# Kernel tuning notes

Measured on AMD Instinct MI355X. Metric: run time of the kernel, lower is better.

## Reference

```python
import math
import jax, jax.numpy as jnp
import numpy as np

N_HEAD = 16
ROPE_BASE = 10000.0


def _rope_tables(T, half, dtype):
    # build_sin_cos(seq_len, dim=head_dim//2): inv freq of length `half`
    pos = jnp.arange(T, dtype=jnp.float32)[:, None]                       # (T,1)
    inv = jnp.exp(jnp.arange(0, 2 * half, 2, dtype=jnp.float32) * (-math.log(ROPE_BASE) / (2 * half)))
    ang = pos * inv                                                        # (T, half)
    return jnp.sin(ang).astype(dtype), jnp.cos(ang).astype(dtype)


def _apply_rope(q, k, sin, cos):
    # q,k: (B,T,H,Dh); sin,cos: (T, Dh//2) -> broadcast over batch and heads
    half = q.shape[-1] // 2
    s = sin[None, :, None, :]
    c = cos[None, :, None, :]
    q1, q2 = q[..., :half], q[..., half:]
    k1, k2 = k[..., :half], k[..., half:]
    q = jnp.concatenate([q1 * c - q2 * s, q2 * c + q1 * s], axis=-1)
    k = jnp.concatenate([k1 * c - k2 * s, k2 * c + k1 * s], axis=-1)
    return q, k


def setup_inputs() -> dict:
    key = jax.random.key(0)
    k1, k2, k3 = jax.random.split(key, 3)
    B, T, C = 2, 2048, 2048
    x = jax.random.normal(k1, (B, T, C), dtype=jnp.float32)
    w_qkv = jax.random.normal(k2, (3 * C, C), dtype=jnp.float32) * (1.0 / math.sqrt(C))
    w_proj = jax.random.normal(k3, (C, C), dtype=jnp.float32) * (1.0 / math.sqrt(C))
    return {"x": x, "w_qkv": w_qkv, "w_proj": w_proj}


def reference(x, w_qkv, w_proj):
    B, T, C = x.shape
    H = N_HEAD
    Dh = C // H
    # fused QKV projection (Linear, no bias): (B,T,3C) -> (B,T,3,H,Dh)
    qkv = jnp.einsum('btc,oc->bto', x, w_qkv).reshape(B, T, 3, H, Dh)
    q, k, v = qkv[:, :, 0], qkv[:, :, 1], qkv[:, :, 2]          # (B,T,H,Dh)
    sin, cos = _rope_tables(T, Dh // 2, x.dtype)
    q, k = _apply_rope(q, k, sin, cos)
    # causal attention, scale 1/sqrt(Dh) (flash default softmax_scale=None)
    scale = 1.0 / math.sqrt(Dh)
    scores = jnp.einsum('bqhd,bkhd->bhqk', q, k) * scale        # (B,H,T,T)
    mask = jnp.tril(jnp.ones((T, T), dtype=bool))
    scores = jnp.where(mask[None, None], scores, jnp.finfo(scores.dtype).min)
    probs = jax.nn.softmax(scores, axis=-1)
    out = jnp.einsum('bhqk,bkhd->bqhd', probs, v)               # (B,T,H,Dh)
    # faithful to original: permute(0,2,1,3) then reshape_as(x)
    out = jnp.transpose(out, (0, 2, 1, 3)).reshape(B, T, C)
    return jnp.einsum('btc,oc->bto', out, w_proj)
```

## Files before the change

kernel.cpp:

```cpp
#include <hip/hip_runtime.h>
#include <hip/hip_bf16.h>

typedef __bf16 bf16_t;
typedef __bf16 bf16x8 __attribute__((ext_vector_type(8)));
typedef __bf16 bf16x4 __attribute__((ext_vector_type(4)));
typedef float f32x4 __attribute__((ext_vector_type(4)));
typedef float f32x16 __attribute__((ext_vector_type(16)));
typedef unsigned u32x4v __attribute__((ext_vector_type(4)));

#define MFMA16(a, b, c) __builtin_amdgcn_mfma_f32_16x16x32_bf16(a, b, c, 0, 0, 0)
#define MFMA32(a, b, c) __builtin_amdgcn_mfma_f32_32x32x16_bf16(a, b, c, 0, 0, 0)

__device__ __forceinline__ void async_copy16(const void* g, void* l) {
  __builtin_amdgcn_global_load_lds(
      (const __attribute__((address_space(1))) void*)g,
      (__attribute__((address_space(3))) void*)l, 16, 0, 0);
}

__device__ __forceinline__ unsigned cvtpk(float lo, float hi) {
  unsigned r;
  asm("v_cvt_pk_bf16_f32 %0, %1, %2" : "=v"(r) : "v"(lo), "v"(hi));
  return r;
}

__global__ void cast_all(const float* __restrict__ x, const float* __restrict__ wqkv,
                         const float* __restrict__ wproj, bf16_t* __restrict__ xb,
                         bf16_t* __restrict__ wqkvb, bf16_t* __restrict__ wprojb) {
  int stride = gridDim.x * blockDim.x;
  for (int i = blockIdx.x * blockDim.x + threadIdx.x; i < 3145728; i += stride) {
    const float* src;
    bf16_t* dst;
    int idx;
    if (i < 1048576) { src = x; dst = xb; idx = i; }
    else if (i < 2621440) { src = wqkv; dst = wqkvb; idx = i - 1048576; }
    else { src = wproj; dst = wprojb; idx = i - 2621440; }
    const float* p = src + (size_t)idx * 8;
    f32x4 a = *(const f32x4*)p;
    f32x4 b = *(const f32x4*)(p + 4);
    bf16x8 o;
    o[0] = (bf16_t)a[0]; o[1] = (bf16_t)a[1]; o[2] = (bf16_t)a[2]; o[3] = (bf16_t)a[3];
    o[4] = (bf16_t)b[0]; o[5] = (bf16_t)b[1]; o[6] = (bf16_t)b[2]; o[7] = (bf16_t)b[3];
    *(bf16x8*)(dst + (size_t)idx * 8) = o;
  }
}

__global__ __launch_bounds__(512, 2) void gemm_qkv(
    const bf16_t* __restrict__ A, const bf16_t* __restrict__ Bw,
    bf16_t* __restrict__ qo, bf16_t* __restrict__ ko,
    int K) {
  __shared__ __align__(16) char lds[131072];
  int tid = threadIdx.x;
  int w = tid >> 6, lane = tid & 63;
  int wm = w & 1, wn = w >> 1;
  int mr = lane & 15, kg = lane >> 4;

  int orig = blockIdx.x;
  int chunk = orig & 7, i = orig >> 3;
  int by = (chunk & 3) * 4 + (i & 3);
  int bx = (chunk >> 2) * 8 + (i >> 2);
  int row0 = by * 256, col0 = bx * 256;

  int lr = tid >> 3, ch = (tid & 7) ^ (lr & 7);
  size_t aoff[4], boff[4];
#pragma unroll
  for (int g = 0; g < 4; ++g) {
    int gr = g * 32 + (lr & 31) + (lr >> 5) * 128;
    aoff[g] = (size_t)(row0 + gr) * K + ch * 8;
  }
#pragma unroll
  for (int p = 0; p < 4; ++p) {
    int gr = (lr >> 4) * 64 + p * 16 + (lr & 15);
    boff[p] = (size_t)(col0 + gr) * K + ch * 8;
  }

  auto stgA = [&](int q, int g, int kt) {
    async_copy16(A + aoff[g] + kt * 64, lds + q * 65536 + g * 8192 + tid * 16);
  };
  auto stgB = [&](int q, int p, int kt) {
    async_copy16(Bw + boff[p] + kt * 64, lds + q * 65536 + 32768 + p * 8192 + tid * 16);
  };

  f32x4 zero = {0.f, 0.f, 0.f, 0.f};
  f32x4 acc[8][4];
#pragma unroll
  for (int mi = 0; mi < 8; ++mi)
#pragma unroll
    for (int ni = 0; ni < 4; ++ni) acc[mi][ni] = zero;

  int nt = K >> 6;

  stgB(0, 0, 0); stgB(0, 1, 0); stgB(0, 2, 0); stgB(0, 3, 0);
  stgA(0, 0, 0); stgA(0, 1, 0); stgA(0, 2, 0); stgA(0, 3, 0);
  asm volatile("s_waitcnt vmcnt(0)" ::: "memory");
  __builtin_amdgcn_sched_barrier(0);
  __builtin_amdgcn_s_barrier();
  __builtin_amdgcn_sched_barrier(0);

#pragma unroll 1
  for (int t = 0; t < nt; ++t) {
    int q = t & 1, qn = q ^ 1;
    int kt = (t + 1 < nt) ? (t + 1) : t;
    const char* Ab = lds + q * 65536;
    const char* Bb = Ab + 32768;
    bf16x8 bf[4][2];

#define QKV_PHASE(MI0, STG, DOWAIT)                                             \
    {                                                                           \
      int r0 = ((MI0) >> 1) * 64 + wm * 32 + mr;                                \
      int r1 = r0 + 16;                                                         \
      bf16x8 a00 = *(const bf16x8*)(Ab + r0 * 128 + ((kg * 16) ^ ((r0 & 7) << 4)));      \
      bf16x8 a01 = *(const bf16x8*)(Ab + r0 * 128 + ((64 + kg * 16) ^ ((r0 & 7) << 4))); \
      bf16x8 a10 = *(const bf16x8*)(Ab + r1 * 128 + ((kg * 16) ^ ((r1 & 7) << 4)));      \
      bf16x8 a11 = *(const bf16x8*)(Ab + r1 * 128 + ((64 + kg * 16) ^ ((r1 & 7) << 4))); \
      STG;                                                                      \
      __builtin_amdgcn_sched_barrier(0);                                        \
      if (DOWAIT) { asm volatile("s_waitcnt vmcnt(4)" ::: "memory"); }          \
      __builtin_amdgcn_s_barrier();                                             \
      asm volatile("s_waitcnt lgkmcnt(0)" ::: "memory");                        \
      __builtin_amdgcn_sched_barrier(0);                                        \
      __builtin_amdgcn_s_setprio(1);                                            \
      _Pragma("unroll")                                                         \
      for (int ni = 0; ni < 4; ++ni) {                                          \
        acc[MI0][ni] = MFMA16(a00, bf[ni][0], acc[MI0][ni]);                    \
        acc[MI0][ni] = MFMA16(a01, bf[ni][1], acc[MI0][ni]);                    \
        acc[(MI0) + 1][ni] = MFMA16(a10, bf[ni][0], acc[(MI0) + 1][ni]);        \
        acc[(MI0) + 1][ni] = MFMA16(a11, bf[ni][1], acc[(MI0) + 1][ni]);        \
      }                                                                         \
      __builtin_amdgcn_s_setprio(0);                                            \
      __builtin_amdgcn_sched_barrier(0);                                        \
      __builtin_amdgcn_s_barrier();                                             \
      __builtin_amdgcn_sched_barrier(0);                                        \
    }

#pragma unroll
    for (int ni = 0; ni < 4; ++ni) {
      int rb = ni * 64 + wn * 16 + mr;
      bf[ni][0] = *(const bf16x8*)(Bb + rb * 128 + ((kg * 16) ^ ((rb & 7) << 4)));
      bf[ni][1] = *(const bf16x8*)(Bb + rb * 128 + ((64 + kg * 16) ^ ((rb & 7) << 4)));
    }
    QKV_PHASE(0, (stgA(qn, 0, kt), stgA(qn, 1, kt), stgB(qn, 0, kt), stgB(qn, 1, kt)), 1)
    QKV_PHASE(2, (stgA(qn, 2, kt), stgA(qn, 3, kt), stgB(qn, 2, kt), stgB(qn, 3, kt)), 0)
    QKV_PHASE(4, (void)0, 0)
    QKV_PHASE(6, (void)0, 0)
#undef QKV_PHASE
  }
  asm volatile("s_waitcnt vmcnt(0)" ::: "memory");
  __syncthreads();

  char* tb = &lds[0];
  int s = col0 >> 11;
  int h0 = (col0 >> 7) & 15;
  int b = row0 >> 11, t0 = row0 & 2047;
#pragma unroll
  for (int mi = 0; mi < 8; ++mi)
#pragma unroll
    for (int ni = 0; ni < 4; ++ni)
#pragma unroll
      for (int jj = 0; jj < 4; ++jj) {
        int rl = wm * 128 + mi * 16 + kg * 4 + jj;
        int cb = (wn * 64 + ni * 16 + mr) * 2;
        *(bf16_t*)(tb + rl * 512 + (cb ^ ((rl & 7) << 4))) = (bf16_t)acc[mi][ni][jj];
      }
  __syncthreads();
  int r = tid >> 1, hs = tid & 1;
  const char* rowb = tb + r * 512;
  int sz = (r & 7) << 4;
  int t = t0 + r;
  bf16_t* dst = (s == 0 ? qo : ko) + ((size_t)((b * 16 + h0 + hs) * 2048 + t)) * 128;
  float tf = (float)t;
  const float cinv = -0.20762050593046014f;
  float postm = (s == 0) ? 0.12751744f : 1.0f;
  bf16x8 vin[16];
#pragma unroll
  for (int m = 0; m < 16; ++m)
    vin[m] = *(const bf16x8*)(rowb + ((hs * 256 + m * 16) ^ sz));
#pragma unroll
  for (int m = 0; m < 8; ++m) {
    bf16x8 o1, o2;
#pragma unroll
    for (int e = 0; e < 8; ++e) {
      float ang = tf * exp2f((float)(m * 8 + e) * cinv);
      float sv = __sinf(ang), cv = __cosf(ang);
      float x1 = (float)vin[m][e], x2 = (float)vin[m + 8][e];
      o1[e] = (bf16_t)((x1 * cv - x2 * sv) * postm);
      o2[e] = (bf16_t)((x2 * cv + x1 * sv) * postm);
    }
    *(bf16x8*)(dst + m * 8) = o1;
    *(bf16x8*)(dst + 64 + m * 8) = o2;
  }
}

template <int MODE>
__global__ __launch_bounds__(512, 2) void gemm256(
    const bf16_t* __restrict__ A, const bf16_t* __restrict__ Bw, float* __restrict__ C,
    bf16_t* __restrict__ vto, int M, int N, int K, int nby, int colbase) {
  __shared__ __align__(16) char lds[147456];
  int tid = threadIdx.x;
  int w = tid >> 6, lane = tid & 63;
  int wm = w >> 1, wn = w & 1;
  int mr = lane & 15, kg = lane >> 4;

  int nwg = gridDim.x;
  int orig = blockIdx.x;
  int wgid = (orig & 7) * (nwg >> 3) + (orig >> 3);
  int by = wgid % nby, bx = wgid / nby;
  int row0 = by * 256, col0 = colbase + bx * 128;

  size_t aoff[4], boff[2];
#pragma unroll
  for (int it = 0; it < 4; ++it) {
    int c = tid + it * 512;
    int r = c >> 3;
    int chs = (c & 7) ^ (r & 7);
    aoff[it] = (size_t)(row0 + r) * K + chs * 8;
  }
#pragma unroll
  for (int it = 0; it < 2; ++it) {
    int c = tid + it * 512;
    int r = c >> 3;
    int chs = (c & 7) ^ (r & 7);
    boff[it] = (size_t)(col0 - colbase + r) * K + chs * 8;
  }

  auto stageA = [&](int buf, int kt, int half) {
    char* Ad = &lds[buf * 49152];
#pragma unroll
    for (int it = half * 2; it < half * 2 + 2; ++it)
      async_copy16(A + aoff[it] + kt * 64, Ad + (tid + it * 512) * 16);
  };
  auto stageB = [&](int buf, int kt) {
    char* Bd = &lds[buf * 49152 + 32768];
#pragma unroll
    for (int it = 0; it < 2; ++it)
      async_copy16(Bw + boff[it] + kt * 64, Bd + (tid + it * 512) * 16);
  };

  f32x4 zero = {0.f, 0.f, 0.f, 0.f};
  f32x4 acc[4][4];
#pragma unroll
  for (int mi = 0; mi < 4; ++mi)
#pragma unroll
    for (int ni = 0; ni < 4; ++ni) acc[mi][ni] = zero;

  int nt = K >> 6;
  stageA(0, 0, 0); stageA(0, 0, 1); stageB(0, 0);
  stageA(1, 1, 0); stageA(1, 1, 1); stageB(1, 1);
  asm volatile("s_waitcnt vmcnt(6)" ::: "memory");
  __builtin_amdgcn_sched_barrier(0);
  __builtin_amdgcn_s_barrier();
  __builtin_amdgcn_sched_barrier(0);

#pragma unroll 1
  for (int t = 0; t < nt; ++t) {
    int cur = t % 3;
    int nxt = (t + 2) % 3;
    int kt2 = (t + 2 < nt) ? (t + 2) : t;
    const char* Ab = &lds[cur * 49152];
    const char* Bb = &lds[cur * 49152 + 32768];
    bf16x8 af[4][2], bfr[4][2];
#pragma unroll
    for (int mi = 0; mi < 4; ++mi) {
      int row = wm * 64 + mi * 16 + mr;
      const char* rb = Ab + row * 128;
      int sz = (row & 7) << 4;
      af[mi][0] = *(const bf16x8*)(rb + ((kg * 16) ^ sz));
      af[mi][1] = *(const bf16x8*)(rb + ((64 + kg * 16) ^ sz));
    }
#pragma unroll
    for (int ni = 0; ni < 4; ++ni) {
      int row = wn * 64 + ni * 16 + mr;
      const char* rb = Bb + row * 128;
      int sz = (row & 7) << 4;
      bfr[ni][0] = *(const bf16x8*)(rb + ((kg * 16) ^ sz));
      bfr[ni][1] = *(const bf16x8*)(rb + ((64 + kg * 16) ^ sz));
    }
    stageA(nxt, kt2, 0);
    __builtin_amdgcn_s_setprio(1);
#pragma unroll
    for (int mi = 0; mi < 4; ++mi) {
      acc[mi][0] = MFMA16(af[mi][0], bfr[0][0], acc[mi][0]);
      acc[mi][0] = MFMA16(af[mi][1], bfr[0][1], acc[mi][0]);
    }
    __builtin_amdgcn_s_setprio(0);
    stageA(nxt, kt2, 1);
    __builtin_amdgcn_s_setprio(1);
#pragma unroll
    for (int mi = 0; mi < 4; ++mi) {
      acc[mi][1] = MFMA16(af[mi][0], bfr[1][0], acc[mi][1]);
      acc[mi][1] = MFMA16(af[mi][1], bfr[1][1], acc[mi][1]);
    }
    __builtin_amdgcn_s_setprio(0);
    stageB(nxt, kt2);
    __builtin_amdgcn_s_setprio(1);
#pragma unroll
    for (int mi = 0; mi < 4; ++mi) {
      acc[mi][2] = MFMA16(af[mi][0], bfr[2][0], acc[mi][2]);
      acc[mi][2] = MFMA16(af[mi][1], bfr[2][1], acc[mi][2]);
      acc[mi][3] = MFMA16(af[mi][0], bfr[3][0], acc[mi][3]);
      acc[mi][3] = MFMA16(af[mi][1], bfr[3][1], acc[mi][3]);
    }
    __builtin_amdgcn_s_setprio(0);
    asm volatile("s_waitcnt vmcnt(6)" ::: "memory");
    __builtin_amdgcn_sched_barrier(0);
    __builtin_amdgcn_s_barrier();
    __builtin_amdgcn_sched_barrier(0);
  }
  asm volatile("s_waitcnt vmcnt(0)" ::: "memory");
  __syncthreads();

  if (MODE == 0) {
#pragma unroll
    for (int mi = 0; mi < 4; ++mi)
#pragma unroll
      for (int ni = 0; ni < 4; ++ni)
#pragma unroll
        for (int jj = 0; jj < 4; ++jj) {
          int row = row0 + wm * 64 + mi * 16 + kg * 4 + jj;
          int col = col0 + wn * 64 + ni * 16 + mr;
          C[(size_t)row * N + col] = acc[mi][ni][jj];
        }
  } else {
    char* tb = &lds[0];
    int h = (col0 >> 7) & 15;
    int b = row0 >> 11, t0 = row0 & 2047;
#pragma unroll
    for (int mi = 0; mi < 4; ++mi)
#pragma unroll
      for (int ni = 0; ni < 4; ++ni)
#pragma unroll
        for (int jj = 0; jj < 4; ++jj) {
          int rloc = wm * 64 + mi * 16 + kg * 4 + jj;
          int cloc = wn * 64 + ni * 16 + mr;
          *(bf16_t*)(tb + cloc * 512 + ((rloc * 2) ^ ((cloc & 7) << 4))) =
              (bf16_t)acc[mi][ni][jj];
        }
    __syncthreads();
    int d = tid >> 2, qt = tid & 3;
    const char* rowb = tb + d * 512;
    int sz = (d & 7) << 4;
    bf16_t* dst = vto + ((size_t)((b * 16 + h) * 128 + d)) * 2048 + t0 + qt * 64;
#pragma unroll
    for (int m2 = 0; m2 < 8; ++m2)
      *(bf16x8*)(dst + m2 * 8) = *(const bf16x8*)(rowb + ((qt * 128 + m2 * 16) ^ sz));
  }
}

__global__ __launch_bounds__(256, 2) void attn_kernel(
    const bf16_t* __restrict__ qg, const bf16_t* __restrict__ kgl,
    const bf16_t* __restrict__ vtg, bf16_t* __restrict__ og) {
  __shared__ __align__(16) bf16_t Ks[2][64 * 128];
  __shared__ __align__(16) bf16_t Vs[2][128 * 64];
  const int T = 2048;
  int tid = threadIdx.x;
  int w = tid >> 6, lane = tid & 63;
  int l31 = lane & 31, hi = lane >> 5;

  int L = blockIdx.x;
  int halfg = L >> 8;
  int Lr = L & 255;
  int role = (Lr & 7) * 32 + (Lr >> 3);
  int bx = role & 7, bh = role >> 3;
  int qb = halfg ? bx : (15 - bx);

  const bf16_t* Q = qg + (size_t)bh * T * 128;
  const bf16_t* K = kgl + (size_t)bh * T * 128;
  const bf16_t* Vt = vtg + (size_t)bh * 128 * T;

  int sb = tid * 16;
  int krl = sb >> 8;
  int kc = (sb & 255) ^ (krl << 4);
  size_t ksrc = (size_t)krl * 128 + (kc >> 1);
  int vdl = sb >> 7;
  int vc = (sb & 127) ^ ((vdl & 7) << 4);
  size_t vsrc = (size_t)vdl * 2048 + (vc >> 1);

  auto stage = [&](int buf, int kb) {
#pragma unroll
    for (int it = 0; it < 4; ++it)
      async_copy16(K + (size_t)(kb + it * 16) * 128 + ksrc, &Ks[buf][it * 2048 + tid * 8]);
#pragma unroll
    for (int it = 0; it < 4; ++it)
      async_copy16(Vt + (size_t)it * 65536 + kb + vsrc, &Vs[buf][it * 2048 + tid * 8]);
  };

  int b = bh >> 4, h = bh & 15;
  f32x16 zero16 = {0.f};
  int swzK = (l31 & 15) << 4;
  int swzV = (l31 & 7) << 4;

  int qw0 = qb * 128 + w * 32;
  int tq = qw0 + l31;
  const bf16_t* qrow = Q + (size_t)tq * 128 + hi * 8;
  bf16x8 qf[8];
#pragma unroll
  for (int dc = 0; dc < 8; ++dc) qf[dc] = *(const bf16x8*)(qrow + dc * 16);

  f32x16 acc[4];
#pragma unroll
  for (int dt = 0; dt < 4; ++dt) acc[dt] = zero16;
  float mrun = -1e30f, lpart = 0.f;

  int nj = 2 * qb + 2;
  stage(0, 0);
  stage(1, 64);
#pragma unroll 1
  for (int j = 0; j < nj; ++j) {
    int cur = j & 1;
    if (j + 1 < nj) {
      asm volatile("s_waitcnt vmcnt(8)" ::: "memory");
    } else {
      asm volatile("s_waitcnt vmcnt(0)" ::: "memory");
    }
    __builtin_amdgcn_sched_barrier(0);
    __syncthreads();
    int kb = j * 64;
    if (kb <= qw0) {
      const char* KsB = (const char*)&Ks[cur][0];
      const char* VsB = (const char*)&Vs[cur][0];
      f32x16 s0 = zero16, s1 = zero16;
      __builtin_amdgcn_s_setprio(1);
#pragma unroll
      for (int dc = 0; dc < 8; ++dc) {
        int cb = dc * 32 + hi * 16;
        bf16x8 k0 = *(const bf16x8*)(KsB + l31 * 256 + (cb ^ swzK));
        bf16x8 k1 = *(const bf16x8*)(KsB + (32 + l31) * 256 + (cb ^ swzK));
        s0 = MFMA32(k0, qf[dc], s0);
        s1 = MFMA32(k1, qf[dc], s1);
      }
      __builtin_amdgcn_s_setprio(0);
      float p0[16], p1[16];
      float lmax = -3e38f;
      bool diag = (kb + 63 > qw0);
#pragma unroll
      for (int r = 0; r < 16; ++r) {
        int kk = (r & 3) + 8 * (r >> 2) + 4 * hi;
        float v0 = s0[r], v1 = s1[r];
        if (diag) {
          if (kb + kk > tq) v0 = -1e30f;
          if (kb + 32 + kk > tq) v1 = -1e30f;
        }
        p0[r] = v0; p1[r] = v1;
        lmax = fmaxf(lmax, fmaxf(v0, v1));
      }
      bool ok = (lmax <= mrun + 8.0f);
      if (!__all(ok)) {
        float tmax = fmaxf(lmax, __shfl_xor(lmax, 32, 64));
        float mn = fmaxf(mrun, tmax);
        float corr = __builtin_amdgcn_exp2f(mrun - mn);
        mrun = mn;
        lpart *= corr;
#pragma unroll
        for (int dt = 0; dt < 4; ++dt)
#pragma unroll
          for (int r = 0; r < 16; ++r) acc[dt][r] *= corr;
      }
#pragma unroll
      for (int r = 0; r < 16; ++r) {
        float e0 = __builtin_amdgcn_exp2f(p0[r] - mrun);
        float e1 = __builtin_amdgcn_exp2f(p1[r] - mrun);
        p0[r] = e0; p1[r] = e1;
        lpart += e0 + e1;
      }
      bf16x8 pa0, pa1, pa2, pa3;
#define BUILD_PA(dst, P, B0)                                         \
      { unsigned a0 = cvtpk(P[(B0) + 0], P[(B0) + 1]);               \
        unsigned a1 = cvtpk(P[(B0) + 2], P[(B0) + 3]);               \
        unsigned b0 = cvtpk(P[(B0) + 4], P[(B0) + 5]);               \
        unsigned b1 = cvtpk(P[(B0) + 6], P[(B0) + 7]);               \
        unsigned xa0 = __shfl_xor(a0, 32, 64);                       \
        unsigned xa1 = __shfl_xor(a1, 32, 64);                       \
        unsigned xb0 = __shfl_xor(b0, 32, 64);                       \
        unsigned xb1 = __shfl_xor(b1, 32, 64);                       \
        u32x4v fw;                                                   \
        fw[0] = hi ? xb0 : a0; fw[1] = hi ? xb1 : a1;                \
        fw[2] = hi ? b0 : xa0; fw[3] = hi ? b1 : xa1;                \
        dst = __builtin_bit_cast(bf16x8, fw); }
      BUILD_PA(pa0, p0, 0)
      BUILD_PA(pa1, p0, 8)
      BUILD_PA(pa2, p1, 0)
      BUILD_PA(pa3, p1, 8)
#undef BUILD_PA
      __builtin_amdgcn_s_setprio(1);
#pragma unroll
      for (int dt = 0; dt < 4; ++dt) {
        const char* vrow = VsB + (dt * 32 + l31) * 128;
        bf16x8 v0 = *(const bf16x8*)(vrow + ((hi * 16) ^ swzV));
        bf16x8 v1 = *(const bf16x8*)(vrow + ((32 + hi * 16) ^ swzV));
        bf16x8 v2 = *(const bf16x8*)(vrow + ((64 + hi * 16) ^ swzV));
        bf16x8 v3 = *(const bf16x8*)(vrow + ((96 + hi * 16) ^ swzV));
        acc[dt] = MFMA32(v0, pa0, acc[dt]);
        acc[dt] = MFMA32(v1, pa1, acc[dt]);
        acc[dt] = MFMA32(v2, pa2, acc[dt]);
        acc[dt] = MFMA32(v3, pa3, acc[dt]);
      }
      __builtin_amdgcn_s_setprio(0);
    }
    __syncthreads();
    if (j + 2 < nj) stage(cur, (j + 2) * 64);
  }
  float l = lpart + __shfl_xor(lpart, 32, 64);
  float invl = 1.0f / l;
  size_t orow_idx = (size_t)b * 2048 + h * 128 + (tq >> 4);
  bf16_t* orow = og + orow_idx * 2048 + (tq & 15) * 128;
#pragma unroll
  for (int dt = 0; dt < 4; ++dt)
#pragma unroll
    for (int g = 0; g < 4; ++g) {
      bf16x4 v4;
#pragma unroll
      for (int e = 0; e < 4; ++e) v4[e] = (bf16_t)(acc[dt][4 * g + e] * invl);
      *(bf16x4*)(orow + dt * 32 + 8 * g + 4 * hi) = v4;
    }
}

extern "C" void kernel_launch(void* const* d_in, const int* in_sizes, int n_in,
                              void* d_out, int out_size, void* d_ws, size_t ws_size,
                              hipStream_t stream) {
  const float* x = (const float*)d_in[0];
  const float* wqkv = (const float*)d_in[1];
  const float* wproj = (const float*)d_in[2];
  float* out = (float*)d_out;
  char* ws = (char*)d_ws;

  const size_t OFF_WQKV = 16777216;
  const size_t OFF_WPROJ = 41943040;
  const size_t OFF_Q = 50331648;
  const size_t OFF_K = 67108864;
  const size_t OFF_VT = 83886080;

  bf16_t* xb = (bf16_t*)(ws);
  bf16_t* wqkvb = (bf16_t*)(ws + OFF_WQKV);
  bf16_t* wprojb = (bf16_t*)(ws + OFF_WPROJ);
  bf16_t* g_q = (bf16_t*)(ws + OFF_Q);
  bf16_t* g_k = (bf16_t*)(ws + OFF_K);
  bf16_t* g_vt = (bf16_t*)(ws + OFF_VT);
  bf16_t* g_att = (bf16_t*)(ws);

  cast_all<<<4096, 256, 0, stream>>>(x, wqkv, wproj, xb, wqkvb, wprojb);
  gemm_qkv<<<256, 512, 0, stream>>>(xb, wqkvb, g_q, g_k, 2048);
  gemm256<1><<<256, 512, 0, stream>>>(xb, wqkvb + (size_t)4096 * 2048, nullptr, g_vt,
                                      4096, 2048, 2048, 16, 4096);
  attn_kernel<<<512, 256, 0, stream>>>(g_q, g_k, g_vt, g_att);
  gemm256<0><<<256, 512, 0, stream>>>(g_att, wprojb, out, nullptr, 4096, 2048, 2048, 16, 0);
}
```

Measured before the change: 243.3 us.

## Merge QK-rope GEMM and V-transpose GEMM into one fused launch

Combines the Q/K projection kernel (with RoPE epilogue) and the V projection kernel (with transposed store) into a single 512-block launch that branches on block index. This removes one kernel launch and the tail/idle gap between the two GEMMs, letting the V blocks fill CUs left idle by the QK grid. The fused kernel uses 147KB LDS and launch bounds of 1 block per CU, so occupancy follows the larger footprint and the two paths now share register allocation.

```diff
diff --git a/kernel.cpp b/kernel.cpp
--- a/kernel.cpp
+++ b/kernel.cpp
@@ -44,282 +44,261 @@
   }
 }
 
-__global__ __launch_bounds__(512, 2) void gemm_qkv(
+__global__ __launch_bounds__(512, 1) void gemm_fused(
     const bf16_t* __restrict__ A, const bf16_t* __restrict__ Bw,
-    bf16_t* __restrict__ qo, bf16_t* __restrict__ ko,
+    bf16_t* __restrict__ qo, bf16_t* __restrict__ ko, bf16_t* __restrict__ vto,
     int K) {
-  __shared__ __align__(16) char lds[131072];
-  int tid = threadIdx.x;
-  int w = tid >> 6, lane = tid & 63;
-  int wm = w & 1, wn = w >> 1;
-  int mr = lane & 15, kg = lane >> 4;
-
-  int orig = blockIdx.x;
-  int chunk = orig & 7, i = orig >> 3;
-  int by = (chunk & 3) * 4 + (i & 3);
-  int bx = (chunk >> 2) * 8 + (i >> 2);
-  int row0 = by * 256, col0 = bx * 256;
-
-  int lr = tid >> 3, ch = (tid & 7) ^ (lr & 7);
-  size_t aoff[4], boff[4];
-#pragma unroll
-  for (int g = 0; g < 4; ++g) {
-    int gr = g * 32 + (lr & 31) + (lr >> 5) * 128;
-    aoff[g] = (size_t)(row0 + gr) * K + ch * 8;
-  }
-#pragma unroll
-  for (int p = 0; p < 4; ++p) {
-    int gr = (lr >> 4) * 64 + p * 16 + (lr & 15);
-    boff[p] = (size_t)(col0 + gr) * K + ch * 8;
-  }
-
-  auto stgA = [&](int q, int g, int kt) {
-    async_copy16(A + aoff[g] + kt * 64, lds + q * 65536 + g * 8192 + tid * 16);
-  };
-  auto stgB = [&](int q, int p, int kt) {
-    async_copy16(Bw + boff[p] + kt * 64, lds + q * 65536 + 32768 + p * 8192 + tid * 16);
-  };
-
-  f32x4 zero = {0.f, 0.f, 0.f, 0.f};
-  f32x4 acc[8][4];
-#pragma unroll
-  for (int mi = 0; mi < 8; ++mi)
-#pragma unroll
-    for (int ni = 0; ni < 4; ++ni) acc[mi][ni] = zero;
-
-  int nt = K >> 6;
-
-  stgB(0, 0, 0); stgB(0, 1, 0); stgB(0, 2, 0); stgB(0, 3, 0);
-  stgA(0, 0, 0); stgA(0, 1, 0); stgA(0, 2, 0); stgA(0, 3, 0);
-  asm volatile("s_waitcnt vmcnt(0)" ::: "memory");
-  __builtin_amdgcn_sched_barrier(0);
-  __builtin_amdgcn_s_barrier();
-  __builtin_amdgcn_sched_barrier(0);
-
-#pragma unroll 1
-  for (int t = 0; t < nt; ++t) {
-    int q = t & 1, qn = q ^ 1;
-    int kt = (t + 1 < nt) ? (t + 1) : t;
-    const char* Ab = lds + q * 65536;
-    const char* Bb = Ab + 32768;
-    bf16x8 bf[4][2];
-
-#define QKV_PHASE(MI0, STG, DOWAIT)                                             \
-    {                                                                           \
-      int r0 = ((MI0) >> 1) * 64 + wm * 32 + mr;                                \
-      int r1 = r0 + 16;                                                         \
-      bf16x8 a00 = *(const bf16x8*)(Ab + r0 * 128 + ((kg * 16) ^ ((r0 & 7) << 4)));      \
-      bf16x8 a01 = *(const bf16x8*)(Ab + r0 * 128 + ((64 + kg * 16) ^ ((r0 & 7) << 4))); \
-      bf16x8 a10 = *(const bf16x8*)(Ab + r1 * 128 + ((kg * 16) ^ ((r1 & 7) << 4)));      \
-      bf16x8 a11 = *(const bf16x8*)(Ab + r1 * 128 + ((64 + kg * 16) ^ ((r1 & 7) << 4))); \
-      STG;                                                                      \
-      __builtin_amdgcn_sched_barrier(0);                                        \
-      if (DOWAIT) { asm volatile("s_waitcnt vmcnt(4)" ::: "memory"); }          \
-      __builtin_amdgcn_s_barrier();                                             \
-      asm volatile("s_waitcnt lgkmcnt(0)" ::: "memory");                        \
-      __builtin_amdgcn_sched_barrier(0);                                        \
-      __builtin_amdgcn_s_setprio(1);                                            \
-      _Pragma("unroll")                                                         \
-      for (int ni = 0; ni < 4; ++ni) {                                          \
-        acc[MI0][ni] = MFMA16(a00, bf[ni][0], acc[MI0][ni]);                    \
-        acc[MI0][ni] = MFMA16(a01, bf[ni][1], acc[MI0][ni]);                    \
-        acc[(MI0) + 1][ni] = MFMA16(a10, bf[ni][0], acc[(MI0) + 1][ni]);        \
-        acc[(MI0) + 1][ni] = MFMA16(a11, bf[ni][1], acc[(MI0) + 1][ni]);        \
-      }                                                                         \
-      __builtin_amdgcn_s_setprio(0);                                            \
-      __builtin_amdgcn_sched_barrier(0);                                        \
-      __builtin_amdgcn_s_barrier();                                             \
-      __builtin_amdgcn_sched_barrier(0);                                        \
-    }
-
-#pragma unroll
-    for (int ni = 0; ni < 4; ++ni) {
-      int rb = ni * 64 + wn * 16 + mr;
-      bf[ni][0] = *(const bf16x8*)(Bb + rb * 128 + ((kg * 16) ^ ((rb & 7) << 4)));
-      bf[ni][1] = *(const bf16x8*)(Bb + rb * 128 + ((64 + kg * 16) ^ ((rb & 7) << 4)));
-    }
-    QKV_PHASE(0, (stgA(qn, 0, kt), stgA(qn, 1, kt), stgB(qn, 0, kt), stgB(qn, 1, kt)), 1)
-    QKV_PHASE(2, (stgA(qn, 2, kt), stgA(qn, 3, kt), stgB(qn, 2, kt), stgB(qn, 3, kt)), 0)
-    QKV_PHASE(4, (void)0, 0)
-    QKV_PHASE(6, (void)0, 0)
-#undef QKV_PHASE
-  }
-  asm volatile("s_waitcnt vmcnt(0)" ::: "memory");
-  __syncthreads();
-
-  char* tb = &lds[0];
-  int s = col0 >> 11;
-  int h0 = (col0 >> 7) & 15;
-  int b = row0 >> 11, t0 = row0 & 2047;
-#pragma unroll
-  for (int mi = 0; mi < 8; ++mi)
-#pragma unroll
-    for (int ni = 0; ni < 4; ++ni)
-#pragma unroll
-      for (int jj = 0; jj < 4; ++jj) {
-        int rl = wm * 128 + mi * 16 + kg * 4 + jj;
-        int cb = (wn * 64 + ni * 16 + mr) * 2;
-        *(bf16_t*)(tb + rl * 512 + (cb ^ ((rl & 7) << 4))) = (bf16_t)acc[mi][ni][jj];
-      }
-  __syncthreads();
-  int r = tid >> 1, hs = tid & 1;
-  const char* rowb = tb + r * 512;
-  int sz = (r & 7) << 4;
-  int t = t0 + r;
-  bf16_t* dst = (s == 0 ? qo : ko) + ((size_t)((b * 16 + h0 + hs) * 2048 + t)) * 128;
-  float tf = (float)t;
-  const float cinv = -0.20762050593046014f;
-  float postm = (s == 0) ? 0.12751744f : 1.0f;
-  bf16x8 vin[16];
-#pragma unroll
-  for (int m = 0; m < 16; ++m)
-    vin[m] = *(const bf16x8*)(rowb + ((hs * 256 + m * 16) ^ sz));
-#pragma unroll
-  for (int m = 0; m < 8; ++m) {
-    bf16x8 o1, o2;
-#pragma unroll
-    for (int e = 0; e < 8; ++e) {
-      float ang = tf * exp2f((float)(m * 8 + e) * cinv);
-      float sv = __sinf(ang), cv = __cosf(ang);
-      float x1 = (float)vin[m][e], x2 = (float)vin[m + 8][e];
-      o1[e] = (bf16_t)((x1 * cv - x2 * sv) * postm);
-      o2[e] = (bf16_t)((x2 * cv + x1 * sv) * postm);
-    }
-    *(bf16x8*)(dst + m * 8) = o1;
-    *(bf16x8*)(dst + 64 + m * 8) = o2;
-  }
-}
-
-template <int MODE>
-__global__ __launch_bounds__(512, 2) void gemm256(
-    const bf16_t* __restrict__ A, const bf16_t* __restrict__ Bw, float* __restrict__ C,
-    bf16_t* __restrict__ vto, int M, int N, int K, int nby, int colbase) {
   __shared__ __align__(16) char lds[147456];
   int tid = threadIdx.x;
   int w = tid >> 6, lane = tid & 63;
-  int wm = w >> 1, wn = w & 1;
   int mr = lane & 15, kg = lane >> 4;
-
-  int nwg = gridDim.x;
-  int orig = blockIdx.x;
-  int wgid = (orig & 7) * (nwg >> 3) + (orig >> 3);
-  int by = wgid % nby, bx = wgid / nby;
-  int row0 = by * 256, col0 = colbase + bx * 128;
-
-  size_t aoff[4], boff[2];
-#pragma unroll
-  for (int it = 0; it < 4; ++it) {
-    int c = tid + it * 512;
-    int r = c >> 3;
-    int chs = (c & 7) ^ (r & 7);
-    aoff[it] = (size_t)(row0 + r) * K + chs * 8;
-  }
-#pragma unroll
-  for (int it = 0; it < 2; ++it) {
-    int c = tid + it * 512;
-    int r = c >> 3;
-    int chs = (c & 7) ^ (r & 7);
-    boff[it] = (size_t)(col0 - colbase + r) * K + chs * 8;
-  }
-
-  auto stageA = [&](int buf, int kt, int half) {
-    char* Ad = &lds[buf * 49152];
-#pragma unroll
-    for (int it = half * 2; it < half * 2 + 2; ++it)
-      async_copy16(A + aoff[it] + kt * 64, Ad + (tid + it * 512) * 16);
-  };
-  auto stageB = [&](int buf, int kt) {
-    char* Bd = &lds[buf * 49152 + 32768];
-#pragma unroll
-    for (int it = 0; it < 2; ++it)
-      async_copy16(Bw + boff[it] + kt * 64, Bd + (tid + it * 512) * 16);
-  };
-
-  f32x4 zero = {0.f, 0.f, 0.f, 0.f};
-  f32x4 acc[4][4];
-#pragma unroll
-  for (int mi = 0; mi < 4; ++mi)
-#pragma unroll
-    for (int ni = 0; ni < 4; ++ni) acc[mi][ni] = zero;
-
-  int nt = K >> 6;
-  stageA(0, 0, 0); stageA(0, 0, 1); stageB(0, 0);
-  stageA(1, 1, 0); stageA(1, 1, 1); stageB(1, 1);
-  asm volatile("s_waitcnt vmcnt(6)" ::: "memory");
-  __builtin_amdgcn_sched_barrier(0);
-  __builtin_amdgcn_s_barrier();
-  __builtin_amdgcn_sched_barrier(0);
+  int bid = blockIdx.x;
+
+  if (bid < 256) {
+    int wm = w & 1, wn = w >> 1;
+    int chunk = bid & 7, i = bid >> 3;
+    int by = (chunk & 3) * 4 + (i & 3);
+    int bx = (chunk >> 2) * 8 + (i >> 2);
+    int row0 = by * 256, col0 = bx * 256;
+
+    int lr = tid >> 3, ch = (tid & 7) ^ (lr & 7);
+    size_t aoff[4], boff[4];
+#pragma unroll
+    for (int g = 0; g < 4; ++g) {
+      int gr = g * 32 + (lr & 31) + (lr >> 5) * 128;
+      aoff[g] = (size_t)(row0 + gr) * K + ch * 8;
+    }
+#pragma unroll
+    for (int p = 0; p < 4; ++p) {
+      int gr = (lr >> 4) * 64 + p * 16 + (lr & 15);
+      boff[p] = (size_t)(col0 + gr) * K + ch * 8;
+    }
+
+    auto stgA = [&](int q, int g, int kt) {
+      async_copy16(A + aoff[g] + kt * 64, lds + q * 65536 + g * 8192 + tid * 16);
+    };
+    auto stgB = [&](int q, int p, int kt) {
+      async_copy16(Bw + boff[p] + kt * 64, lds + q * 65536 + 32768 + p * 8192 + tid * 16);
+    };
+
+    f32x4 zero = {0.f, 0.f, 0.f, 0.f};
+    f32x4 acc[8][4];
+#pragma unroll
+    for (int mi = 0; mi < 8; ++mi)
+#pragma unroll
+      for (int ni = 0; ni < 4; ++ni) acc[mi][ni] = zero;
+
+    int nt = K >> 6;
+
+    stgB(0, 0, 0); stgB(0, 1, 0); stgB(0, 2, 0); stgB(0, 3, 0);
+    stgA(0, 0, 0); stgA(0, 1, 0); stgA(0, 2, 0); stgA(0, 3, 0);
+    asm volatile("s_waitcnt vmcnt(0)" ::: "memory");
+    __builtin_amdgcn_sched_barrier(0);
+    __builtin_amdgcn_s_barrier();
+    __builtin_amdgcn_sched_barrier(0);
 
 #pragma unroll 1
-  for (int t = 0; t < nt; ++t) {
-    int cur = t % 3;
-    int nxt = (t + 2) % 3;
-    int kt2 = (t + 2 < nt) ? (t + 2) : t;
-    const char* Ab = &lds[cur * 49152];
-    const char* Bb = &lds[cur * 49152 + 32768];
-    bf16x8 af[4][2], bfr[4][2];
-#pragma unroll
-    for (int mi = 0; mi < 4; ++mi) {
-      int row = wm * 64 + mi * 16 + mr;
-      const char* rb = Ab + row * 128;
-      int sz = (row & 7) << 4;
-      af[mi][0] = *(const bf16x8*)(rb + ((kg * 16) ^ sz));
-      af[mi][1] = *(const bf16x8*)(rb + ((64 + kg * 16) ^ sz));
-    }
-#pragma unroll
-    for (int ni = 0; ni < 4; ++ni) {
-      int row = wn * 64 + ni * 16 + mr;
-      const char* rb = Bb + row * 128;
-      int sz = (row & 7) << 4;
-      bfr[ni][0] = *(const bf16x8*)(rb + ((kg * 16) ^ sz));
-      bfr[ni][1] = *(const bf16x8*)(rb + ((64 + kg * 16) ^ sz));
-    }
-    stageA(nxt, kt2, 0);
-    __builtin_amdgcn_s_setprio(1);
-#pragma unroll
-    for (int mi = 0; mi < 4; ++mi) {
-      acc[mi][0] = MFMA16(af[mi][0], bfr[0][0], acc[mi][0]);
-      acc[mi][0] = MFMA16(af[mi][1], bfr[0][1], acc[mi][0]);
-    }
-    __builtin_amdgcn_s_setprio(0);
-    stageA(nxt, kt2, 1);
-    __builtin_amdgcn_s_setprio(1);
-#pragma unroll
-    for (int mi = 0; mi < 4; ++mi) {
-      acc[mi][1] = MFMA16(af[mi][0], bfr[1][0], acc[mi][1]);
-      acc[mi][1] = MFMA16(af[mi][1], bfr[1][1], acc[mi][1]);
-    }
-    __builtin_amdgcn_s_setprio(0);
-    stageB(nxt, kt2);
-    __builtin_amdgcn_s_setprio(1);
-#pragma unroll
-    for (int mi = 0; mi < 4; ++mi) {
-      acc[mi][2] = MFMA16(af[mi][0], bfr[2][0], acc[mi][2]);
-      acc[mi][2] = MFMA16(af[mi][1], bfr[2][1], acc[mi][2]);
-      acc[mi][3] = MFMA16(af[mi][0], bfr[3][0], acc[mi][3]);
-      acc[mi][3] = MFMA16(af[mi][1], bfr[3][1], acc[mi][3]);
-    }
-    __builtin_amdgcn_s_setprio(0);
+    for (int t = 0; t < nt; ++t) {
+      int q = t & 1, qn = q ^ 1;
+      int kt = (t + 1 < nt) ? (t + 1) : t;
+      const char* Ab = lds + q * 65536;
+      const char* Bb = Ab + 32768;
+      bf16x8 bf[4][2];
+
+#define QKV_PHASE(MI0, STG, DOWAIT)                                             \
+      {                                                                         \
+        int r0 = ((MI0) >> 1) * 64 + wm * 32 + mr;                              \
+        int r1 = r0 + 16;                                                       \
+        bf16x8 a00 = *(const bf16x8*)(Ab + r0 * 128 + ((kg * 16) ^ ((r0 & 7) << 4)));      \
+        bf16x8 a01 = *(const bf16x8*)(Ab + r0 * 128 + ((64 + kg * 16) ^ ((r0 & 7) << 4))); \
+        bf16x8 a10 = *(const bf16x8*)(Ab + r1 * 128 + ((kg * 16) ^ ((r1 & 7) << 4)));      \
+        bf16x8 a11 = *(const bf16x8*)(Ab + r1 * 128 + ((64 + kg * 16) ^ ((r1 & 7) << 4))); \
+        STG;                                                                    \
+        __builtin_amdgcn_sched_barrier(0);                                      \
+        if (DOWAIT) { asm volatile("s_waitcnt vmcnt(4)" ::: "memory"); }        \
+        __builtin_amdgcn_s_barrier();                                           \
+        asm volatile("s_waitcnt lgkmcnt(0)" ::: "memory");                      \
+        __builtin_amdgcn_sched_barrier(0);                                      \
+        __builtin_amdgcn_s_setprio(1);                                          \
+        _Pragma("unroll")                                                       \
+        for (int ni = 0; ni < 4; ++ni) {                                        \
+          acc[MI0][ni] = MFMA16(a00, bf[ni][0], acc[MI0][ni]);                  \
+          acc[MI0][ni] = MFMA16(a01, bf[ni][1], acc[MI0][ni]);                  \
+          acc[(MI0) + 1][ni] = MFMA16(a10, bf[ni][0], acc[(MI0) + 1][ni]);      \
+          acc[(MI0) + 1][ni] = MFMA16(a11, bf[ni][1], acc[(MI0) + 1][ni]);      \
+        }                                                                       \
+        __builtin_amdgcn_s_setprio(0);                                          \
+        __builtin_amdgcn_sched_barrier(0);                                      \
+        __builtin_amdgcn_s_barrier();                                           \
+        __builtin_amdgcn_sched_barrier(0);                                      \
+      }
+
+#pragma unroll
+      for (int ni = 0; ni < 4; ++ni) {
+        int rb = ni * 64 + wn * 16 + mr;
+        bf[ni][0] = *(const bf16x8*)(Bb + rb * 128 + ((kg * 16) ^ ((rb & 7) << 4)));
+        bf[ni][1] = *(const bf16x8*)(Bb + rb * 128 + ((64 + kg * 16) ^ ((rb & 7) << 4)));
+      }
+      QKV_PHASE(0, (stgA(qn, 0, kt), stgA(qn, 1, kt), stgB(qn, 0, kt), stgB(qn, 1, kt)), 1)
+      QKV_PHASE(2, (stgA(qn, 2, kt), stgA(qn, 3, kt), stgB(qn, 2, kt), stgB(qn, 3, kt)), 0)
+      QKV_PHASE(4, (void)0, 0)
+      QKV_PHASE(6, (void)0, 0)
+#undef QKV_PHASE
+    }
+    asm volatile("s_waitcnt vmcnt(0)" ::: "memory");
+    __syncthreads();
+
+    char* tb = &lds[0];
+    int s = col0 >> 11;
+    int h0 = (col0 >> 7) & 15;
+    int b = row0 >> 11, t0 = row0 & 2047;
+#pragma unroll
+    for (int mi = 0; mi < 8; ++mi)
+#pragma unroll
+      for (int ni = 0; ni < 4; ++ni)
+#pragma unroll
+        for (int jj = 0; jj < 4; ++jj) {
+          int rl = wm * 128 + mi * 16 + kg * 4 + jj;
+          int cb = (wn * 64 + ni * 16 + mr) * 2;
+          *(bf16_t*)(tb + rl * 512 + (cb ^ ((rl & 7) << 4))) = (bf16_t)acc[mi][ni][jj];
+        }
+    __syncthreads();
+    int r = tid >> 1, hs = tid & 1;
+    const char* rowb = tb + r * 512;
+    int sz = (r & 7) << 4;
+    int t = t0 + r;
+    bf16_t* dst = (s == 0 ? qo : ko) + ((size_t)((b * 16 + h0 + hs) * 2048 + t)) * 128;
+    float tf = (float)t;
+    const float cinv = -0.20762050593046014f;
+    float postm = (s == 0) ? 0.12751744f : 1.0f;
+    bf16x8 vin[16];
+#pragma unroll
+    for (int m = 0; m < 16; ++m)
+      vin[m] = *(const bf16x8*)(rowb + ((hs * 256 + m * 16) ^ sz));
+#pragma unroll
+    for (int m = 0; m < 8; ++m) {
+      bf16x8 o1, o2;
+#pragma unroll
+      for (int e = 0; e < 8; ++e) {
+        float ang = tf * exp2f((float)(m * 8 + e) * cinv);
+        float sv = __sinf(ang), cv = __cosf(ang);
+        float x1 = (float)vin[m][e], x2 = (float)vin[m + 8][e];
+        o1[e] = (bf16_t)((x1 * cv - x2 * sv) * postm);
+        o2[e] = (bf16_t)((x2 * cv + x1 * sv) * postm);
+      }
+      *(bf16x8*)(dst + m * 8) = o1;
+      *(bf16x8*)(dst + 64 + m * 8) = o2;
+    }
+  } else {
+    int wm = w >> 1, wn = w & 1;
+    const bf16_t* Bv = Bw + (size_t)4096 * K;
+    int vid = bid - 256;
+    int wgid = (vid & 7) * 32 + (vid >> 3);
+    int by = wgid % 16, bx = wgid / 16;
+    int row0 = by * 256, col0 = 4096 + bx * 128;
+
+    size_t aoff[4], boff[2];
+#pragma unroll
+    for (int it = 0; it < 4; ++it) {
+      int c = tid + it * 512;
+      int r = c >> 3;
+      int chs = (c & 7) ^ (r & 7);
+      aoff[it] = (size_t)(row0 + r) * K + chs * 8;
+    }
+#pragma unroll
+    for (int it = 0; it < 2; ++it) {
+      int c = tid + it * 512;
+      int r = c >> 3;
+      int chs = (c & 7) ^ (r & 7);
+      boff[it] = (size_t)(col0 - 4096 + r) * K + chs * 8;
+    }
+
+    auto stageA = [&](int buf, int kt, int half) {
+      char* Ad = &lds[buf * 49152];
+#pragma unroll
+      for (int it = half * 2; it < half * 2 + 2; ++it)
+        async_copy16(A + aoff[it] + kt * 64, Ad + (tid + it * 512) * 16);
+    };
+    auto stageB = [&](int buf, int kt) {
+      char* Bd = &lds[buf * 49152 + 32768];
+#pragma unroll
+      for (int it = 0; it < 2; ++it)
+        async_copy16(Bv + boff[it] + kt * 64, Bd + (tid + it * 512) * 16);
+    };
+
+    f32x4 zero = {0.f, 0.f, 0.f, 0.f};
+    f32x4 acc[4][4];
+#pragma unroll
+    for (int mi = 0; mi < 4; ++mi)
+#pragma unroll
+      for (int ni = 0; ni < 4; ++ni) acc[mi][ni] = zero;
+
+    int nt = K >> 6;
+    stageA(0, 0, 0); stageA(0, 0, 1); stageB(0, 0);
+    stageA(1, 1, 0); stageA(1, 1, 1); stageB(1, 1);
     asm volatile("s_waitcnt vmcnt(6)" ::: "memory");
     __builtin_amdgcn_sched_barrier(0);
     __builtin_amdgcn_s_barrier();
     __builtin_amdgcn_sched_barrier(0);
-  }
-  asm volatile("s_waitcnt vmcnt(0)" ::: "memory");
-  __syncthreads();
-
-  if (MODE == 0) {
-#pragma unroll
-    for (int mi = 0; mi < 4; ++mi)
-#pragma unroll
-      for (int ni = 0; ni < 4; ++ni)
-#pragma unroll
-        for (int jj = 0; jj < 4; ++jj) {
-          int row = row0 + wm * 64 + mi * 16 + kg * 4 + jj;
-          int col = col0 + wn * 64 + ni * 16 + mr;
-          C[(size_t)row * N + col] = acc[mi][ni][jj];
-        }
-  } else {
+
+#pragma unroll 1
+    for (int t = 0; t < nt; ++t) {
+      int cur = t % 3;
+      int nxt = (t + 2) % 3;
+      int kt2 = (t + 2 < nt) ? (t + 2) : t;
+      const char* Ab = &lds[cur * 49152];
+      const char* Bb = &lds[cur * 49152 + 32768];
+      bf16x8 af[4][2], bfr[4][2];
+#pragma unroll
+      for (int mi = 0; mi < 4; ++mi) {
+        int row = wm * 64 + mi * 16 + mr;
+        const char* rb = Ab + row * 128;
+        int sz = (row & 7) << 4;
+        af[mi][0] = *(const bf16x8*)(rb + ((kg * 16) ^ sz));
+        af[mi][1] = *(const bf16x8*)(rb + ((64 + kg * 16) ^ sz));
+      }
+#pragma unroll
+      for (int ni = 0; ni < 4; ++ni) {
+        int row = wn * 64 + ni * 16 + mr;
+        const char* rb = Bb + row * 128;
+        int sz = (row & 7) << 4;
+        bfr[ni][0] = *(const bf16x8*)(rb + ((kg * 16) ^ sz));
+        bfr[ni][1] = *(const bf16x8*)(rb + ((64 + kg * 16) ^ sz));
+      }
+      stageA(nxt, kt2, 0);
+      __builtin_amdgcn_s_setprio(1);
+#pragma unroll
+      for (int mi = 0; mi < 4; ++mi) {
+        acc[mi][0] = MFMA16(af[mi][0], bfr[0][0], acc[mi][0]);
+        acc[mi][0] = MFMA16(af[mi][1], bfr[0][1], acc[mi][0]);
+      }
+      __builtin_amdgcn_s_setprio(0);
+      stageA(nxt, kt2, 1);
+      __builtin_amdgcn_s_setprio(1);
+#pragma unroll
+      for (int mi = 0; mi < 4; ++mi) {
+        acc[mi][1] = MFMA16(af[mi][0], bfr[1][0], acc[mi][1]);
+        acc[mi][1] = MFMA16(af[mi][1], bfr[1][1], acc[mi][1]);
+      }
+      __builtin_amdgcn_s_setprio(0);
+      stageB(nxt, kt2);
+      __builtin_amdgcn_s_setprio(1);
+#pragma unroll
+      for (int mi = 0; mi < 4; ++mi) {
+        acc[mi][2] = MFMA16(af[mi][0], bfr[2][0], acc[mi][2]);
+        acc[mi][2] = MFMA16(af[mi][1], bfr[2][1], acc[mi][2]);
+        acc[mi][3] = MFMA16(af[mi][0], bfr[3][0], acc[mi][3]);
+        acc[mi][3] = MFMA16(af[mi][1], bfr[3][1], acc[mi][3]);
+      }
+      __builtin_amdgcn_s_setprio(0);
+      asm volatile("s_waitcnt vmcnt(6)" ::: "memory");
+      __builtin_amdgcn_sched_barrier(0);
+      __builtin_amdgcn_s_barrier();
+      __builtin_amdgcn_sched_barrier(0);
+    }
+    asm volatile("s_waitcnt vmcnt(0)" ::: "memory");
+    __syncthreads();
+
     char* tb = &lds[0];
     int h = (col0 >> 7) & 15;
     int b = row0 >> 11, t0 = row0 & 2047;
@@ -343,6 +322,135 @@
     for (int m2 = 0; m2 < 8; ++m2)
       *(bf16x8*)(dst + m2 * 8) = *(const bf16x8*)(rowb + ((qt * 128 + m2 * 16) ^ sz));
   }
+}
+
+__global__ __launch_bounds__(512, 2) void gemm256(
+    const bf16_t* __restrict__ A, const bf16_t* __restrict__ Bw, float* __restrict__ C,
+    int M, int N, int K, int nby) {
+  __shared__ __align__(16) char lds[147456];
+  int tid = threadIdx.x;
+  int w = tid >> 6, lane = tid & 63;
+  int wm = w >> 1, wn = w & 1;
+  int mr = lane & 15, kg = lane >> 4;
+
+  int nwg = gridDim.x;
+  int orig = blockIdx.x;
+  int wgid = (orig & 7) * (nwg >> 3) + (orig >> 3);
+  int by = wgid % nby, bx = wgid / nby;
+  int row0 = by * 256, col0 = bx * 128;
+
+  size_t aoff[4], boff[2];
+#pragma unroll
+  for (int it = 0; it < 4; ++it) {
+    int c = tid + it * 512;
+    int r = c >> 3;
+    int chs = (c & 7) ^ (r & 7);
+    aoff[it] = (size_t)(row0 + r) * K + chs * 8;
+  }
+#pragma unroll
+  for (int it = 0; it < 2; ++it) {
+    int c = tid + it * 512;
+    int r = c >> 3;
+    int chs = (c & 7) ^ (r & 7);
+    boff[it] = (size_t)(col0 + r) * K + chs * 8;
+  }
+
+  auto stageA = [&](int buf, int kt, int half) {
+    char* Ad = &lds[buf * 49152];
+#pragma unroll
+    for (int it = half * 2; it < half * 2 + 2; ++it)
+      async_copy16(A + aoff[it] + kt * 64, Ad + (tid + it * 512) * 16);
+  };
+  auto stageB = [&](int buf, int kt) {
+    char* Bd = &lds[buf * 49152 + 32768];
+#pragma unroll
+    for (int it = 0; it < 2; ++it)
+      async_copy16(Bw + boff[it] + kt * 64, Bd + (tid + it * 512) * 16);
+  };
+
+  f32x4 zero = {0.f, 0.f, 0.f, 0.f};
+  f32x4 acc[4][4];
+#pragma unroll
+  for (int mi = 0; mi < 4; ++mi)
+#pragma unroll
+    for (int ni = 0; ni < 4; ++ni) acc[mi][ni] = zero;
+
+  int nt = K >> 6;
+  stageA(0, 0, 0); stageA(0, 0, 1); stageB(0, 0);
+  stageA(1, 1, 0); stageA(1, 1, 1); stageB(1, 1);
+  asm volatile("s_waitcnt vmcnt(6)" ::: "memory");
+  __builtin_amdgcn_sched_barrier(0);
+  __builtin_amdgcn_s_barrier();
+  __builtin_amdgcn_sched_barrier(0);
+
+#pragma unroll 1
+  for (int t = 0; t < nt; ++t) {
+    int cur = t % 3;
+    int nxt = (t + 2) % 3;
+    int kt2 = (t + 2 < nt) ? (t + 2) : t;
+    const char* Ab = &lds[cur * 49152];
+    const char* Bb = &lds[cur * 49152 + 32768];
+    bf16x8 af[4][2], bfr[4][2];
+#pragma unroll
+    for (int mi = 0; mi < 4; ++mi) {
+      int row = wm * 64 + mi * 16 + mr;
+      const char* rb = Ab + row * 128;
+      int sz = (row & 7) << 4;
+      af[mi][0] = *(const bf16x8*)(rb + ((kg * 16) ^ sz));
+      af[mi][1] = *(const bf16x8*)(rb + ((64 + kg * 16) ^ sz));
+    }
+#pragma unroll
+    for (int ni = 0; ni < 4; ++ni) {
+      int row = wn * 64 + ni * 16 + mr;
+      const char* rb = Bb + row * 128;
+      int sz = (row & 7) << 4;
+      bfr[ni][0] = *(const bf16x8*)(rb + ((kg * 16) ^ sz));
+      bfr[ni][1] = *(const bf16x8*)(rb + ((64 + kg * 16) ^ sz));
+    }
+    stageA(nxt, kt2, 0);
+    __builtin_amdgcn_s_setprio(1);
+#pragma unroll
+    for (int mi = 0; mi < 4; ++mi) {
+      acc[mi][0] = MFMA16(af[mi][0], bfr[0][0], acc[mi][0]);
+      acc[mi][0] = MFMA16(af[mi][1], bfr[0][1], acc[mi][0]);
+    }
+    __builtin_amdgcn_s_setprio(0);
+    stageA(nxt, kt2, 1);
+    __builtin_amdgcn_s_setprio(1);
+#pragma unroll
+    for (int mi = 0; mi < 4; ++mi) {
+      acc[mi][1] = MFMA16(af[mi][0], bfr[1][0], acc[mi][1]);
+      acc[mi][1] = MFMA16(af[mi][1], bfr[1][1], acc[mi][1]);
+    }
+    __builtin_amdgcn_s_setprio(0);
+    stageB(nxt, kt2);
+    __builtin_amdgcn_s_setprio(1);
+#pragma unroll
+    for (int mi = 0; mi < 4; ++mi) {
+      acc[mi][2] = MFMA16(af[mi][0], bfr[2][0], acc[mi][2]);
+      acc[mi][2] = MFMA16(af[mi][1], bfr[2][1], acc[mi][2]);
+      acc[mi][3] = MFMA16(af[mi][0], bfr[3][0], acc[mi][3]);
+      acc[mi][3] = MFMA16(af[mi][1], bfr[3][1], acc[mi][3]);
+    }
+    __builtin_amdgcn_s_setprio(0);
+    asm volatile("s_waitcnt vmcnt(6)" ::: "memory");
+    __builtin_amdgcn_sched_barrier(0);
+    __builtin_amdgcn_s_barrier();
+    __builtin_amdgcn_sched_barrier(0);
+  }
+  asm volatile("s_waitcnt vmcnt(0)" ::: "memory");
+  __syncthreads();
+
+#pragma unroll
+  for (int mi = 0; mi < 4; ++mi)
+#pragma unroll
+    for (int ni = 0; ni < 4; ++ni)
+#pragma unroll
+      for (int jj = 0; jj < 4; ++jj) {
+        int row = row0 + wm * 64 + mi * 16 + kg * 4 + jj;
+        int col = col0 + wn * 64 + ni * 16 + mr;
+        C[(size_t)row * N + col] = acc[mi][ni][jj];
+      }
 }
 
 __global__ __launch_bounds__(256, 2) void attn_kernel(
@@ -537,9 +645,7 @@
   bf16_t* g_att = (bf16_t*)(ws);
 
   cast_all<<<4096, 256, 0, stream>>>(x, wqkv, wproj, xb, wqkvb, wprojb);
-  gemm_qkv<<<256, 512, 0, stream>>>(xb, wqkvb, g_q, g_k, 2048);
-  gemm256<1><<<256, 512, 0, stream>>>(xb, wqkvb + (size_t)4096 * 2048, nullptr, g_vt,
-                                      4096, 2048, 2048, 16, 4096);
+  gemm_fused<<<512, 512, 0, stream>>>(xb, wqkvb, g_q, g_k, g_vt, 2048);
   attn_kernel<<<512, 256, 0, stream>>>(g_q, g_k, g_vt, g_att);
-  gemm256<0><<<256, 512, 0, stream>>>(g_att, wprojb, out, nullptr, 4096, 2048, 2048, 16, 0);
+  gemm256<<<256, 512, 0, stream>>>(g_att, wprojb, out, 4096, 2048, 2048, 16);
 }
```

After: 246.5 us. Within noise of the previous version (+1.3%).
